# Optimization experiments

Hardware: AMD Instinct MI355X
Metric: run time of the kernel (lower is better)

## Reference

```python
import jax, jax.numpy as jnp
import numpy as np

B, QL, KL, D, H = 2, 512, 8192, 1024, 8
HD = D // H  # head dim = 128


def setup_inputs() -> dict:
    key = jax.random.key(0)
    ks = jax.random.split(key, 12)
    s = 0.02
    return {
        "inputs_q": jax.random.normal(ks[0], (B, QL, D), jnp.float32),
        "inputs_k": jax.random.normal(ks[1], (B, KL, D), jnp.float32),
        "inputs_v": jax.random.normal(ks[2], (B, KL, D), jnp.float32),
        "attention_mask": jax.random.randint(ks[3], (B, QL, KL), 0, 2).astype(bool),
        "Wq": jax.random.normal(ks[4], (D, D), jnp.float32) * s,
        "bq": jnp.zeros((D,), jnp.float32),
        "Wk": jax.random.normal(ks[5], (D, D), jnp.float32) * s,
        "bk": jnp.zeros((D,), jnp.float32),
        "Wv": jax.random.normal(ks[6], (D, D), jnp.float32) * s,
        "bv": jnp.zeros((D,), jnp.float32),
        "Wf": jax.random.normal(ks[7], (D, D), jnp.float32) * s,
        "bf": jnp.zeros((D,), jnp.float32),
    }


def reference(inputs_q, inputs_k, inputs_v, attention_mask, Wq, bq, Wk, bk, Wv, bv, Wf, bf):
    # Projections (torch Linear: x @ W.T + b)
    q = inputs_q @ Wq.T + bq  # [B, QL, D]
    k = inputs_k @ Wk.T + bk  # [B, KL, D]
    v = inputs_v @ Wv.T + bv  # [B, KL, D]

    q = q.reshape(B, QL, H, HD)
    k = k.reshape(B, KL, H, HD)
    v = v.reshape(B, KL, H, HD)

    # scores [B, H, QL, KL]
    scores = jnp.einsum("bqhd,bkhd->bhqk", q, k)
    scale = 1.0 / np.sqrt(HD).astype(np.float32)
    scores = scores * scale
    large_k = jnp.float32(1e30)
    scores = jnp.where(attention_mask[:, None, :, :], scores, -large_k)

    probs = jax.nn.softmax(scores, axis=-1)
    # note: original calls self.dropout(normalized) but discards the result -> no-op

    summed = jnp.einsum("bhqk,bkhd->bqhd", probs, v).reshape(B, QL, H * HD)

    # wipe rows whose mask is all zero
    wipe = jnp.all(~attention_mask, axis=2, keepdims=True)  # [B, QL, 1]
    summed = jnp.where(wipe, jnp.zeros_like(summed), summed)

    return summed @ Wf.T + bf
```

## Files before the change

kernel.cpp:

```cpp
#include <hip/hip_runtime.h>
#include <hip/hip_bf16.h>
#include <math.h>

typedef __attribute__((ext_vector_type(4))) float fx4;
typedef __attribute__((ext_vector_type(4))) short sx4;
typedef __attribute__((ext_vector_type(8))) short sx8;
typedef unsigned long long u64;

#define MFMA16(a, b, c) __builtin_amdgcn_mfma_f32_16x16x16bf16_1k(a, b, c, 0, 0, 0)
#define MFMA32(a, b, c) __builtin_amdgcn_mfma_f32_16x16x32_bf16(a, b, c, 0, 0, 0)

__device__ __forceinline__ unsigned short f2bf(float f) {
  unsigned int u = __float_as_uint(f);
  return (unsigned short)((u + 0x7fffu + ((u >> 16) & 1u)) >> 16);
}

typedef const __attribute__((address_space(1))) char* gc1p;
typedef __attribute__((address_space(3))) char* lc3p;
__device__ __forceinline__ void glds16(const void* g, const void* lds_uniform) {
  gc1p gp = (gc1p)(unsigned long long)(uintptr_t)g;
  lc3p lp = (lc3p)(unsigned)__builtin_amdgcn_readfirstlane((int)(unsigned)(uintptr_t)lds_uniform);
  __builtin_amdgcn_global_load_lds(gp, lp, 16, 0, 0);
}

__global__ __launch_bounds__(256) void k_conv(const float* __restrict__ s,
                                              short* __restrict__ d) {
  size_t i = ((size_t)blockIdx.x * 256 + threadIdx.x) * 8;
  const fx4 a = *(const fx4*)(s + i);
  const fx4 b = *(const fx4*)(s + i + 4);
  sx8 o;
  o[0] = (short)f2bf(a[0]); o[1] = (short)f2bf(a[1]);
  o[2] = (short)f2bf(a[2]); o[3] = (short)f2bf(a[3]);
  o[4] = (short)f2bf(b[0]); o[5] = (short)f2bf(b[1]);
  o[6] = (short)f2bf(b[2]); o[7] = (short)f2bf(b[3]);
  *(sx8*)(d + i) = o;
}

__global__ __launch_bounds__(256) void k_conv5(const float* s0, const float* s1,
                                               const float* s2, const float* s3,
                                               const float* s4, short* d0, short* d1,
                                               short* d2, short* d3, short* d4) {
  const int seg = blockIdx.x >> 9;
  const float* s = seg == 0 ? s0 : seg == 1 ? s1 : seg == 2 ? s2 : seg == 3 ? s3 : s4;
  short* d = seg == 0 ? d0 : seg == 1 ? d1 : seg == 2 ? d2 : seg == 3 ? d3 : d4;
  size_t i = ((size_t)(blockIdx.x & 511) * 256 + threadIdx.x) * 8;
  const fx4 a = *(const fx4*)(s + i);
  const fx4 b = *(const fx4*)(s + i + 4);
  sx8 o;
  o[0] = (short)f2bf(a[0]); o[1] = (short)f2bf(a[1]);
  o[2] = (short)f2bf(a[2]); o[3] = (short)f2bf(a[3]);
  o[4] = (short)f2bf(b[0]); o[5] = (short)f2bf(b[1]);
  o[6] = (short)f2bf(b[2]); o[7] = (short)f2bf(b[3]);
  *(sx8*)(d + i) = o;
}

__global__ __launch_bounds__(256) void k_pack_mask(const int* __restrict__ mask,
                                                   u64* __restrict__ mb) {
  int g = blockIdx.x * 256 + threadIdx.x;
  u64 bal = __ballot(mask[g] != 0);
  if ((threadIdx.x & 63) == 0) mb[g >> 6] = bal;
}

template <bool OUT_F32>
__global__ __launch_bounds__(256) void k_gemm(const short* __restrict__ A,
                                              const short* __restrict__ Bw,
                                              const float* __restrict__ bias,
                                              void* __restrict__ Cptr,
                                              int M, int N, int K, float alpha) {
  __shared__ __align__(16) short sA[8192];
  __shared__ __align__(16) short sB[8192];
  const int t = threadIdx.x;
  const int lane = t & 63;
  const int w = t >> 6;
  const int quad = lane >> 4;
  const int l16 = lane & 15;
  const int x7 = l16 & 7;
  const int mt = M >> 7;
  const int m0 = (blockIdx.x % mt) << 7;
  const int n0 = (blockIdx.x / mt) << 7;
  const int wm = (w >> 1) << 6;
  const int wn = (w & 1) << 6;
  const fx4 fzero = {0.f, 0.f, 0.f, 0.f};
  fx4 acc[4][4];
#pragma unroll
  for (int i = 0; i < 4; i++)
#pragma unroll
    for (int j = 0; j < 4; j++) acc[i][j] = fzero;

  const int srow = (lane >> 3);
  const int scb = lane & 7;

  for (int k0 = 0; k0 < K; k0 += 64) {
    __syncthreads();
#pragma unroll
    for (int j = 0; j < 4; j++) {
      const int row = w * 32 + j * 8 + srow;
      const int cb = scb ^ (row & 7);
      glds16(A + (size_t)(m0 + row) * K + k0 + cb * 8, &sA[(w * 32 + j * 8) * 64]);
      glds16(Bw + (size_t)(n0 + row) * K + k0 + cb * 8, &sB[(w * 32 + j * 8) * 64]);
    }
    __syncthreads();
#pragma unroll
    for (int kc = 0; kc < 2; kc++) {
      const int cbp = ((kc * 4 + quad) ^ x7) * 8;
      sx8 fa[4], fb[4];
#pragma unroll
      for (int i = 0; i < 4; i++) {
        fa[i] = *(const sx8*)(&sA[(wm + i * 16 + l16) * 64 + cbp]);
        fb[i] = *(const sx8*)(&sB[(wn + i * 16 + l16) * 64 + cbp]);
      }
#pragma unroll
      for (int mi = 0; mi < 4; mi++)
#pragma unroll
        for (int ni = 0; ni < 4; ni++)
          acc[mi][ni] = MFMA32(fa[mi], fb[ni], acc[mi][ni]);
    }
  }
#pragma unroll
  for (int ni = 0; ni < 4; ni++) {
    const int col = n0 + wn + ni * 16 + l16;
    const float bval = bias[col];
#pragma unroll
    for (int mi = 0; mi < 4; mi++)
#pragma unroll
      for (int r = 0; r < 4; r++) {
        const int row = m0 + wm + mi * 16 + quad * 4 + r;
        const float v = (acc[mi][ni][r] + bval) * alpha;
        if (OUT_F32) ((float*)Cptr)[(size_t)row * N + col] = v;
        else ((unsigned short*)Cptr)[(size_t)row * N + col] = f2bf(v);
      }
  }
}

__global__ __launch_bounds__(256) void k_transpose_v(const short* __restrict__ Vp,
                                                     short* __restrict__ Vt) {
  __shared__ __align__(16) short tile[64 * 72];
  const int x = blockIdx.x;
  const int tm = x & 255;
  const int td = x >> 8;
  const int m0 = tm << 6;
  const int b = m0 >> 13;
  const int kl0 = m0 & 8191;
  const int d0 = td << 6;
  const int t = threadIdx.x;
  const int c = t & 7;
#pragma unroll
  for (int j = 0; j < 2; j++) {
    const int r = (t >> 3) + j * 32;
    *(sx8*)(&tile[r * 72 + c * 8]) = *(const sx8*)(Vp + (size_t)(m0 + r) * 1024 + d0 + c * 8);
  }
  __syncthreads();
#pragma unroll
  for (int j = 0; j < 2; j++) {
    const int d = (t >> 3) + j * 32;
    sx8 v;
#pragma unroll
    for (int i = 0; i < 8; i++) v[i] = tile[(c * 8 + i) * 72 + d];
    *(sx8*)(Vt + (size_t)(b * 1024 + d0 + d) * 8192 + kl0 + c * 8) = v;
  }
}

__global__ __launch_bounds__(256, 4) void k_attn(const short* __restrict__ Qp,
                                                 const short* __restrict__ Kp,
                                                 const short* __restrict__ Vt,
                                                 const u64* __restrict__ mb,
                                                 float* __restrict__ ml,
                                                 float* __restrict__ Op) {
  __shared__ __align__(16) short sK[8192];
  __shared__ __align__(16) short sV[8192];
  const int x = blockIdx.x;
  const int s = x & 7;
  const int qt = (x >> 3) & 7;
  const int h = (x >> 6) & 7;
  const int b = x >> 9;
  const int t = threadIdx.x;
  const int lane = t & 63;
  const int w = t >> 6;
  const int quad = lane >> 4;
  const int l16 = lane & 15;
  const int x7 = l16 & 7;
  const int q0 = qt << 6;
  const fx4 fzero = {0.f, 0.f, 0.f, 0.f};

  const short* qbase = Qp + (size_t)(b * 512 + q0 + w * 16 + l16) * 1024 + h * 128;
  sx8 aq[4];
#pragma unroll
  for (int kc = 0; kc < 4; kc++) aq[kc] = *(const sx8*)(qbase + kc * 32 + quad * 8);

  fx4 Ot[8];
#pragma unroll
  for (int d = 0; d < 8; d++) Ot[d] = fzero;
  float lsum = 0.f;

  const short* kbase = Kp + (size_t)(b * 8192 + s * 1024) * 1024 + h * 128;
  const short* vbase = Vt + (size_t)(b * 1024 + h * 128) * 8192 + s * 1024;
  const u64* wdp = mb + (size_t)(b * 512 + q0 + w * 16 + l16) * 128 + s * 16;
  const int srow4 = lane >> 4, scb16 = lane & 15;
  const int srow8 = lane >> 3, scb8 = lane & 7;

  for (int kt = 0; kt < 16; kt++) {
    __syncthreads();
#pragma unroll
    for (int j = 0; j < 4; j++) {
      const int row = (w * 4 + j) * 4 + srow4;
      const int cb = scb16 ^ (row & 7);
      glds16(kbase + (size_t)(kt * 64 + row) * 1024 + cb * 8, &sK[(w * 4 + j) * 512]);
    }
#pragma unroll
    for (int j = 0; j < 4; j++) {
      const int row = (w * 4 + j) * 8 + srow8;
      const int cb = scb8 ^ (row & 7);
      glds16(vbase + (size_t)row * 8192 + kt * 64 + cb * 8, &sV[(w * 4 + j) * 512]);
    }
    const u64 wd = wdp[kt];
    __syncthreads();
    const unsigned lo = (unsigned)wd, hi = (unsigned)(wd >> 32);
    sx4 pk[4];
#pragma unroll
    for (int nt = 0; nt < 4; nt++) {
      fx4 a = fzero;
#pragma unroll
      for (int kc = 0; kc < 4; kc++) {
        const sx8 kf = *(const sx8*)(&sK[(nt * 16 + l16) * 128 + ((kc * 4 + quad) ^ x7) * 8]);
        a = MFMA32(kf, aq[kc], a);
      }
      const unsigned bits = (nt & 2) ? hi : lo;
      const int sh = (nt & 1) * 16 + quad * 4;
      sx4 pko;
#pragma unroll
      for (int r = 0; r < 4; r++) {
        const float e = exp2f(a[r]);
        const float p = ((bits >> (sh + r)) & 1u) ? e : 0.f;
        lsum += p;
        pko[r] = (short)f2bf(p);
      }
      pk[nt] = pko;
    }
#pragma unroll
    for (int dt = 0; dt < 8; dt++) {
      fx4 o = Ot[dt];
#pragma unroll
      for (int nt = 0; nt < 4; nt++) {
        const int cb = (2 * nt + (quad >> 1)) ^ x7;
        const sx4 vf = *(const sx4*)(&sV[(dt * 16 + l16) * 64 + cb * 8 + (quad & 1) * 4]);
        o = MFMA16(vf, pk[nt], o);
      }
      Ot[dt] = o;
    }
  }
  lsum += __shfl_xor(lsum, 16, 64);
  lsum += __shfl_xor(lsum, 32, 64);
  if (lane < 16) ml[(size_t)x * 64 + w * 16 + l16] = lsum;
  float* ob = Op + (size_t)x * 8192 + (w * 16 + l16) * 128 + quad * 4;
#pragma unroll
  for (int dt = 0; dt < 8; dt++) *(fx4*)(ob + dt * 16) = Ot[dt];
}

__global__ __launch_bounds__(256) void k_combine(const float* __restrict__ ml,
                                                 const float* __restrict__ Op,
                                                 short* __restrict__ summed) {
  const int xc = blockIdx.x;
  const int qt = xc & 7;
  const int h = (xc >> 3) & 7;
  const int b = xc >> 6;
  const int t = threadIdx.x;
  const int row = t >> 2;
  const int dg = (t & 3) * 32;
  float L = 0.f;
#pragma unroll
  for (int s = 0; s < 8; s++) L += ml[(size_t)(xc * 8 + s) * 64 + row];
  float o[32];
#pragma unroll
  for (int i = 0; i < 32; i++) o[i] = 0.f;
  if (L != 0.f) {
#pragma unroll
    for (int s = 0; s < 8; s++) {
      const float* src = Op + (size_t)(xc * 8 + s) * 8192 + row * 128 + dg;
#pragma unroll
      for (int i = 0; i < 8; i++) {
        const fx4 v = *(const fx4*)(src + i * 4);
        o[i * 4 + 0] += v[0]; o[i * 4 + 1] += v[1];
        o[i * 4 + 2] += v[2]; o[i * 4 + 3] += v[3];
      }
    }
    const float inv = 1.f / L;
#pragma unroll
    for (int i = 0; i < 32; i++) o[i] *= inv;
  }
  short* dst = summed + (size_t)(b * 512 + qt * 64 + row) * 1024 + h * 128 + dg;
#pragma unroll
  for (int i = 0; i < 4; i++) {
    sx8 pkv;
#pragma unroll
    for (int j = 0; j < 8; j++) pkv[j] = (short)f2bf(o[i * 8 + j]);
    *(sx8*)(dst + i * 8) = pkv;
  }
}

extern "C" void kernel_launch(void* const* d_in, const int* in_sizes, int n_in,
                              void* d_out, int out_size, void* d_ws, size_t ws_size,
                              hipStream_t stream) {
  (void)in_sizes; (void)n_in; (void)out_size; (void)ws_size;
  const float* inq = (const float*)d_in[0];
  const float* ink = (const float*)d_in[1];
  const float* inv = (const float*)d_in[2];
  const int* mask = (const int*)d_in[3];
  const float* Wq = (const float*)d_in[4];
  const float* bq = (const float*)d_in[5];
  const float* Wk = (const float*)d_in[6];
  const float* bk = (const float*)d_in[7];
  const float* Wv = (const float*)d_in[8];
  const float* bv = (const float*)d_in[9];
  const float* Wf = (const float*)d_in[10];
  const float* bf = (const float*)d_in[11];

  char* ws = (char*)d_ws;
  short* S1 = (short*)(ws + 0);
  short* S2 = (short*)(ws + 33554432);
  short* S3 = (short*)(ws + 67108864);
  short* cq = (short*)(ws + 100663296);
  short* cwq = (short*)(ws + 102760448);
  short* cwk = (short*)(ws + 104857600);
  short* cwv = (short*)(ws + 106954752);
  short* cwf = (short*)(ws + 109051904);
  short* Qp = (short*)(ws + 111149056);
  short* summed = (short*)(ws + 113246208);
  u64* mb = (u64*)(ws + 115343360);
  float* ml = (float*)(ws + 116391936);

  const float alpha_q = 0.12751757f;

  k_conv5<<<2560, 256, 0, stream>>>(inq, Wq, Wk, Wv, Wf, cq, cwq, cwk, cwv, cwf);
  k_pack_mask<<<32768, 256, 0, stream>>>(mask, mb);
  k_conv<<<8192, 256, 0, stream>>>(ink, S1);
  k_gemm<false><<<1024, 256, 0, stream>>>(S1, cwk, bk, S2, 16384, 1024, 1024, 1.f);
  k_conv<<<8192, 256, 0, stream>>>(inv, S1);
  k_gemm<false><<<1024, 256, 0, stream>>>(S1, cwv, bv, S3, 16384, 1024, 1024, 1.f);
  k_gemm<false><<<64, 256, 0, stream>>>(cq, cwq, bq, Qp, 1024, 1024, 1024, alpha_q);
  k_transpose_v<<<4096, 256, 0, stream>>>(S3, S1);
  k_attn<<<1024, 256, 0, stream>>>(Qp, S2, S1, mb, ml, (float*)S3);
  k_combine<<<128, 256, 0, stream>>>(ml, (const float*)S3, summed);
  k_gemm<true><<<64, 256, 0, stream>>>(summed, cwf, bf, (float*)d_out, 1024, 1024, 1024, 1.f);
}
```

Baseline: 436.7 us.

## Fuse V transpose into V-projection epilogue and merge conversion kernels

The V projection GEMM now writes its bf16 output directly in the transposed [B, D, KL] layout, with a small XOR swizzle on the key index. This removes the separate transpose kernel and its full read/write of V, and the attention kernel's V fragment reads are adjusted to match the swizzle. The K-input conversion is merged into the weight conversion launch. Other changes: the GEMM tile ordering now walks N fastest, and softmax bf16 packing uses a perm-based round-half-up instead of round-to-nearest-even. The transposed epilogue makes scattered 8-byte stores, and the rounding change alters numerics slightly.

```diff
diff --git a/kernel.cpp b/kernel.cpp
--- a/kernel.cpp
+++ b/kernel.cpp
@@ -36,14 +36,25 @@
   *(sx8*)(d + i) = o;
 }
 
-__global__ __launch_bounds__(256) void k_conv5(const float* s0, const float* s1,
-                                               const float* s2, const float* s3,
-                                               const float* s4, short* d0, short* d1,
-                                               short* d2, short* d3, short* d4) {
-  const int seg = blockIdx.x >> 9;
-  const float* s = seg == 0 ? s0 : seg == 1 ? s1 : seg == 2 ? s2 : seg == 3 ? s3 : s4;
-  short* d = seg == 0 ? d0 : seg == 1 ? d1 : seg == 2 ? d2 : seg == 3 ? d3 : d4;
-  size_t i = ((size_t)(blockIdx.x & 511) * 256 + threadIdx.x) * 8;
+__global__ __launch_bounds__(256) void k_conv_a(const float* ink, const float* inq,
+                                                const float* Wq, const float* Wk,
+                                                const float* Wv, const float* Wf,
+                                                short* ck, short* cq, short* cwq,
+                                                short* cwk, short* cwv, short* cwf) {
+  int bx = blockIdx.x;
+  const float* s;
+  short* d;
+  size_t i;
+  if (bx < 8192) {
+    s = ink; d = ck; i = (size_t)bx * 2048;
+  } else {
+    const int r = bx - 8192;
+    const int seg = r >> 9;
+    s = seg == 0 ? inq : seg == 1 ? Wq : seg == 2 ? Wk : seg == 3 ? Wv : Wf;
+    d = seg == 0 ? cq : seg == 1 ? cwq : seg == 2 ? cwk : seg == 3 ? cwv : cwf;
+    i = (size_t)(r & 511) * 2048;
+  }
+  i += (size_t)threadIdx.x * 8;
   const fx4 a = *(const fx4*)(s + i);
   const fx4 b = *(const fx4*)(s + i + 4);
   sx8 o;
@@ -61,7 +72,7 @@
   if ((threadIdx.x & 63) == 0) mb[g >> 6] = bal;
 }
 
-template <bool OUT_F32>
+template <int MODE>
 __global__ __launch_bounds__(256) void k_gemm(const short* __restrict__ A,
                                               const short* __restrict__ Bw,
                                               const float* __restrict__ bias,
@@ -75,9 +86,9 @@
   const int quad = lane >> 4;
   const int l16 = lane & 15;
   const int x7 = l16 & 7;
-  const int mt = M >> 7;
-  const int m0 = (blockIdx.x % mt) << 7;
-  const int n0 = (blockIdx.x / mt) << 7;
+  const int ntile = N >> 7;
+  const int n0 = (blockIdx.x % ntile) << 7;
+  const int m0 = (blockIdx.x / ntile) << 7;
   const int wm = (w >> 1) << 6;
   const int wn = (w & 1) << 6;
   const fx4 fzero = {0.f, 0.f, 0.f, 0.f};
@@ -120,43 +131,28 @@
   for (int ni = 0; ni < 4; ni++) {
     const int col = n0 + wn + ni * 16 + l16;
     const float bval = bias[col];
-#pragma unroll
-    for (int mi = 0; mi < 4; mi++)
-#pragma unroll
-      for (int r = 0; r < 4; r++) {
-        const int row = m0 + wm + mi * 16 + quad * 4 + r;
-        const float v = (acc[mi][ni][r] + bval) * alpha;
-        if (OUT_F32) ((float*)Cptr)[(size_t)row * N + col] = v;
-        else ((unsigned short*)Cptr)[(size_t)row * N + col] = f2bf(v);
-      }
-  }
-}
-
-__global__ __launch_bounds__(256) void k_transpose_v(const short* __restrict__ Vp,
-                                                     short* __restrict__ Vt) {
-  __shared__ __align__(16) short tile[64 * 72];
-  const int x = blockIdx.x;
-  const int tm = x & 255;
-  const int td = x >> 8;
-  const int m0 = tm << 6;
-  const int b = m0 >> 13;
-  const int kl0 = m0 & 8191;
-  const int d0 = td << 6;
-  const int t = threadIdx.x;
-  const int c = t & 7;
-#pragma unroll
-  for (int j = 0; j < 2; j++) {
-    const int r = (t >> 3) + j * 32;
-    *(sx8*)(&tile[r * 72 + c * 8]) = *(const sx8*)(Vp + (size_t)(m0 + r) * 1024 + d0 + c * 8);
-  }
-  __syncthreads();
-#pragma unroll
-  for (int j = 0; j < 2; j++) {
-    const int d = (t >> 3) + j * 32;
-    sx8 v;
-#pragma unroll
-    for (int i = 0; i < 8; i++) v[i] = tile[(c * 8 + i) * 72 + d];
-    *(sx8*)(Vt + (size_t)(b * 1024 + d0 + d) * 8192 + kl0 + c * 8) = v;
+    if (MODE == 2) {
+#pragma unroll
+      for (int mi = 0; mi < 4; mi++) {
+        const int rowb = m0 + wm + mi * 16 + quad * 4;
+        const int bb = rowb >> 13;
+        const int kl = (rowb & 8191) ^ ((col & 8) ? 4 : 0);
+        sx4 pkv;
+#pragma unroll
+        for (int r = 0; r < 4; r++) pkv[r] = (short)f2bf(acc[mi][ni][r] + bval);
+        *(sx4*)((unsigned short*)Cptr + ((size_t)bb * 1024 + col) * 8192 + kl) = pkv;
+      }
+    } else {
+#pragma unroll
+      for (int mi = 0; mi < 4; mi++)
+#pragma unroll
+        for (int r = 0; r < 4; r++) {
+          const int row = m0 + wm + mi * 16 + quad * 4 + r;
+          const float v = (acc[mi][ni][r] + bval) * alpha;
+          if (MODE == 1) ((float*)Cptr)[(size_t)row * N + col] = v;
+          else ((unsigned short*)Cptr)[(size_t)row * N + col] = f2bf(v);
+        }
+    }
   }
 }
 
@@ -197,6 +193,7 @@
   const u64* wdp = mb + (size_t)(b * 512 + q0 + w * 16 + l16) * 128 + s * 16;
   const int srow4 = lane >> 4, scb16 = lane & 15;
   const int srow8 = lane >> 3, scb8 = lane & 7;
+  const int h4 = ((quad & 1) ^ ((l16 >> 3) & 1)) * 4;
 
   for (int kt = 0; kt < 16; kt++) {
     __syncthreads();
@@ -226,14 +223,18 @@
       }
       const unsigned bits = (nt & 2) ? hi : lo;
       const int sh = (nt & 1) * 16 + quad * 4;
+      float pv[4];
+#pragma unroll
+      for (int r = 0; r < 4; r++) {
+        const float e = __builtin_amdgcn_exp2f(a[r]);
+        pv[r] = ((bits >> (sh + r)) & 1u) ? e : 0.f;
+        lsum += pv[r];
+      }
       sx4 pko;
-#pragma unroll
-      for (int r = 0; r < 4; r++) {
-        const float e = exp2f(a[r]);
-        const float p = ((bits >> (sh + r)) & 1u) ? e : 0.f;
-        lsum += p;
-        pko[r] = (short)f2bf(p);
-      }
+      ((unsigned*)&pko)[0] = __builtin_amdgcn_perm(
+          __float_as_uint(pv[1]) + 0x8000u, __float_as_uint(pv[0]) + 0x8000u, 0x07060302u);
+      ((unsigned*)&pko)[1] = __builtin_amdgcn_perm(
+          __float_as_uint(pv[3]) + 0x8000u, __float_as_uint(pv[2]) + 0x8000u, 0x07060302u);
       pk[nt] = pko;
     }
 #pragma unroll
@@ -242,7 +243,7 @@
 #pragma unroll
       for (int nt = 0; nt < 4; nt++) {
         const int cb = (2 * nt + (quad >> 1)) ^ x7;
-        const sx4 vf = *(const sx4*)(&sV[(dt * 16 + l16) * 64 + cb * 8 + (quad & 1) * 4]);
+        const sx4 vf = *(const sx4*)(&sV[(dt * 16 + l16) * 64 + cb * 8 + h4]);
         o = MFMA16(vf, pk[nt], o);
       }
       Ot[dt] = o;
@@ -330,15 +331,13 @@
 
   const float alpha_q = 0.12751757f;
 
-  k_conv5<<<2560, 256, 0, stream>>>(inq, Wq, Wk, Wv, Wf, cq, cwq, cwk, cwv, cwf);
+  k_conv_a<<<10752, 256, 0, stream>>>(ink, inq, Wq, Wk, Wv, Wf, S1, cq, cwq, cwk, cwv, cwf);
   k_pack_mask<<<32768, 256, 0, stream>>>(mask, mb);
-  k_conv<<<8192, 256, 0, stream>>>(ink, S1);
-  k_gemm<false><<<1024, 256, 0, stream>>>(S1, cwk, bk, S2, 16384, 1024, 1024, 1.f);
+  k_gemm<0><<<1024, 256, 0, stream>>>(S1, cwk, bk, S2, 16384, 1024, 1024, 1.f);
   k_conv<<<8192, 256, 0, stream>>>(inv, S1);
-  k_gemm<false><<<1024, 256, 0, stream>>>(S1, cwv, bv, S3, 16384, 1024, 1024, 1.f);
-  k_gemm<false><<<64, 256, 0, stream>>>(cq, cwq, bq, Qp, 1024, 1024, 1024, alpha_q);
-  k_transpose_v<<<4096, 256, 0, stream>>>(S3, S1);
-  k_attn<<<1024, 256, 0, stream>>>(Qp, S2, S1, mb, ml, (float*)S3);
-  k_combine<<<128, 256, 0, stream>>>(ml, (const float*)S3, summed);
-  k_gemm<true><<<64, 256, 0, stream>>>(summed, cwf, bf, (float*)d_out, 1024, 1024, 1024, 1.f);
-}
+  k_gemm<2><<<1024, 256, 0, stream>>>(S1, cwv, bv, S3, 16384, 1024, 1024, 1.f);
+  k_gemm<0><<<64, 256, 0, stream>>>(cq, cwq, bq, Qp, 1024, 1024, 1024, alpha_q);
+  k_attn<<<1024, 256, 0, stream>>>(Qp, S2, S3, mb, ml, (float*)S1);
+  k_combine<<<128, 256, 0, stream>>>(ml, (const float*)S1, summed);
+  k_gemm<1><<<64, 256, 0, stream>>>(summed, cwf, bf, (float*)d_out, 1024, 1024, 1024, 1.f);
+}
```

Measured after the change: 428.1 us. Within noise of the previous version (-2.0%).
